# Performance work log

Hardware: AMD Instinct MI355X
Metric: run time of the kernel (lower is better)

Reference implementation:

```python
import jax, jax.numpy as jnp
import numpy as np
from jax import lax

B, S, I, H = 64, 512, 1024, 1024


def _lstm_dir(x, W_ih, W_hh, b_ih, b_hh):
    # x: [B, S, I] -> hidden states [B, S, H]
    # Precompute input projections for all timesteps in one GEMM.
    xg = jnp.einsum('bsi,gi->bsg', x, W_ih) + b_ih + b_hh  # [B, S, 4H]
    Whh_T = W_hh.T  # [H, 4H]
    h0 = jnp.zeros((x.shape[0], W_hh.shape[1]), dtype=x.dtype)
    c0 = jnp.zeros_like(h0)

    def step(carry, xg_t):
        h, c = carry
        g = xg_t + h @ Whh_T  # [B, 4H]
        i_g, f_g, g_g, o_g = jnp.split(g, 4, axis=-1)  # PyTorch gate order i,f,g,o
        i_g = jax.nn.sigmoid(i_g)
        f_g = jax.nn.sigmoid(f_g)
        g_g = jnp.tanh(g_g)
        o_g = jax.nn.sigmoid(o_g)
        c = f_g * c + i_g * g_g
        h = o_g * jnp.tanh(c)
        return (h, c), h

    _, hs = lax.scan(step, (h0, c0), jnp.swapaxes(xg, 0, 1))  # hs: [S, B, H]
    return jnp.swapaxes(hs, 0, 1)


def setup_inputs() -> dict:
    key = jax.random.key(0)
    ks = jax.random.split(key, 10)
    s = 1.0 / np.sqrt(H)  # PyTorch LSTMCell init scale
    return {
        'forward_x': jax.random.normal(ks[0], (B, S, I), jnp.float32),
        'backward_x': jax.random.normal(ks[1], (B, S, I), jnp.float32),
        'W_ih_f': jax.random.uniform(ks[2], (4 * H, I), jnp.float32, -s, s),
        'W_hh_f': jax.random.uniform(ks[3], (4 * H, H), jnp.float32, -s, s),
        'b_ih_f': jax.random.uniform(ks[4], (4 * H,), jnp.float32, -s, s),
        'b_hh_f': jax.random.uniform(ks[5], (4 * H,), jnp.float32, -s, s),
        'W_ih_b': jax.random.uniform(ks[6], (4 * H, I), jnp.float32, -s, s),
        'W_hh_b': jax.random.uniform(ks[7], (4 * H, H), jnp.float32, -s, s),
        'b_ih_b': jax.random.uniform(ks[8], (4 * H,), jnp.float32, -s, s),
        'b_hh_b': jax.random.uniform(ks[9], (4 * H,), jnp.float32, -s, s),
    }


def reference(forward_x, backward_x, W_ih_f, W_hh_f, b_ih_f, b_hh_f,
              W_ih_b, W_hh_b, b_ih_b, b_hh_b):
    fwd = _lstm_dir(forward_x, W_ih_f, W_hh_f, b_ih_f, b_hh_f)
    # Backward direction consumes backward_x from the last timestep to the
    # first and writes hidden states back at their original positions,
    # i.e. run on the time-reversed sequence and reverse the outputs.
    bwd = _lstm_dir(backward_x[:, ::-1, :], W_ih_b, W_hh_b, b_ih_b, b_hh_b)[:, ::-1, :]
    return fwd, bwd
```

## Files before the change

kernel.cpp:

```cpp
#include <hip/hip_runtime.h>
#include <hip/hip_bf16.h>
#include <cstdint>


typedef __bf16 bf16_t;
typedef bf16_t bf16x8 __attribute__((ext_vector_type(8)));
typedef float  f32x4  __attribute__((ext_vector_type(4)));
typedef int    i32x2  __attribute__((ext_vector_type(2)));

#define DEVI __device__ __forceinline__

constexpr int Bb = 64, Ss = 512, Ii = 1024, Hh = 1024;
constexpr size_t WS_FLAGS  = 0;
constexpr size_t WS_HRING  = 4096;
constexpr size_t WS_XBF    = 1ull << 20;
constexpr size_t XBF_BYTES = 2ull * Ss * Bb * Ii * 2;
constexpr size_t WS_NEED_XBF = WS_XBF + XBF_BYTES;
constexpr int LDS_TOTAL = 163840;

DEVI float fast_sig(float x) {
  float z = __expf(-fabsf(x));
  float r = __builtin_amdgcn_rcpf(1.f + z);
  return x >= 0.f ? r : z * r;
}
DEVI float fast_tanh(float x) {
  float z = __expf(-2.f * fabsf(x));
  float r = (1.f - z) * __builtin_amdgcn_rcpf(1.f + z);
  return x >= 0.f ? r : -r;
}
DEVI bf16x8 cvt8(f32x4 a, f32x4 b) {
  bf16x8 r;
  r[0] = (bf16_t)a[0]; r[1] = (bf16_t)a[1]; r[2] = (bf16_t)a[2]; r[3] = (bf16_t)a[3];
  r[4] = (bf16_t)b[0]; r[5] = (bf16_t)b[1]; r[6] = (bf16_t)b[2]; r[7] = (bf16_t)b[3];
  return r;
}
DEVI uint32_t pk_bf16(float lo, float hi) {
  union { bf16_t b[2]; uint32_t u; } x;
  x.b[0] = (bf16_t)lo; x.b[1] = (bf16_t)hi;
  return x.u;
}
DEVI f32x4 mfma16(bf16x8 a, bf16x8 b, f32x4 c) {
  return __builtin_amdgcn_mfma_f32_16x16x32_bf16(a, b, c, 0, 0, 0);
}

#define GLDS16(g, s)                                                           \
  __builtin_amdgcn_global_load_lds(                                            \
      (const __attribute__((address_space(1))) void*)(const void*)(g),         \
      (__attribute__((address_space(3))) void*)(void*)(s), 16, 0, 0)
#define GLDS16_COH(g, s)                                                       \
  __builtin_amdgcn_global_load_lds(                                            \
      (const __attribute__((address_space(1))) void*)(const void*)(g),         \
      (__attribute__((address_space(3))) void*)(void*)(s), 16, 0, 17)
#define WAIT_LGKM0 asm volatile("s_waitcnt lgkmcnt(0)" ::: "memory")
#define WAIT_VM0   asm volatile("s_waitcnt vmcnt(0)" ::: "memory")
#define BARRIER_RAW                                                            \
  do { __builtin_amdgcn_s_barrier(); __builtin_amdgcn_sched_barrier(0); } while (0)

__global__ void k_init(int* flags) {
  int i = threadIdx.x;
  if (i < 256) flags[i] = 0;
}

__global__ void k_convx(const float* __restrict__ xf, const float* __restrict__ xb,
                        bf16_t* __restrict__ dst) {
  size_t og = (size_t)blockIdx.x * blockDim.x + threadIdx.x;
  int i8  = (int)(og & 127);
  int b   = (int)((og >> 7) & 63);
  int t   = (int)((og >> 13) & 511);
  int dir = (int)(og >> 22);
  const float* src = (dir ? xb : xf) + (((size_t)b * Ss + t) * Ii + (size_t)i8 * 8);
  f32x4 a = *(const f32x4*)src;
  f32x4 c = *(const f32x4*)(src + 4);
  *(bf16x8*)(dst + og * 8) = cvt8(a, c);
}

template <bool XBF>
__global__ void __launch_bounds__(512, 2)
k_lstm(const float* __restrict__ xf, const float* __restrict__ xb,
       const float* __restrict__ Wih_f, const float* __restrict__ Whh_f,
       const float* __restrict__ bih_f, const float* __restrict__ bhh_f,
       const float* __restrict__ Wih_b, const float* __restrict__ Whh_b,
       const float* __restrict__ bih_b, const float* __restrict__ bhh_b,
       float* __restrict__ out,
       const bf16_t* __restrict__ xbfin, bf16_t* __restrict__ hring,
       int* __restrict__ flags) {
  extern __shared__ char lds[];
  char* PA = lds;
  char* PB = lds + 65536;
  float* part = (float*)(lds + 131072);

  const int tid = threadIdx.x;
  const int bid = blockIdx.x;
  const int dir = bid & 1;
  const int db  = bid >> 1;
  const int n0  = db * 8;
  const int w   = tid >> 6, l = tid & 63;
  const int u   = l >> 4, l15 = l & 15;
  const int m   = w & 1;
  const int kq  = w >> 1;

  const float* Wih = dir ? Wih_b : Wih_f;
  const float* Whh = dir ? Whh_b : Whh_f;
  const float* bih = dir ? bih_b : bih_f;
  const float* bhh = dir ? bhh_b : bhh_f;
  const float* x32 = dir ? xb : xf;
  const bf16_t* xbase = xbfin + (size_t)dir * Ss * Bb * Ii;
  bf16_t* hr = hring + (size_t)dir * 2 * Bb * Hh;
  float* outD = out + (size_t)dir * Bb * Ss * Hh;
  int* myflags = flags + dir * 128;

  bf16x8 wr[2][2][4][2];
#pragma unroll
  for (int mat = 0; mat < 2; ++mat)
#pragma unroll
    for (int p = 0; p < 2; ++p)
#pragma unroll
      for (int ks = 0; ks < 4; ++ks)
#pragma unroll
        for (int nt = 0; nt < 2; ++nt) {
          int c = nt * 16 + l15;
          int j = (c >> 3) * 1024 + n0 + (c & 7);
          int k = p * 512 + kq * 128 + ks * 32 + u * 8;
          const float* sp = (mat ? Whh : Wih) + (size_t)j * 1024 + k;
          wr[mat][p][ks][nt] = cvt8(*(const f32x4*)sp, *(const f32x4*)(sp + 4));
        }

  const int eb = tid >> 3, en = tid & 7;
  const int nj = n0 + en;
  float bi0 = bih[nj] + bhh[nj];
  float bi1 = bih[1024 + nj] + bhh[1024 + nj];
  float bi2 = bih[2048 + nj] + bhh[2048 + nj];
  float bi3 = bih[3072 + nj] + bhh[3072 + nj];

  int aoff0[4], aoff1[4];
#pragma unroll
  for (int ks = 0; ks < 4; ++ks) {
    int r0 = m * 32 + l15;
    int r1 = r0 + 16;
    int sl = kq * 16 + ks * 4 + u;
    aoff0[ks] = r0 * 1024 + ((sl ^ (r0 & 7)) << 4);
    aoff1[ks] = r1 * 1024 + ((sl ^ (r1 & 7)) << 4);
  }

  auto STAGE_DMA = [&](char* panel, const bf16_t* srcb) {
#pragma unroll
    for (int i = 0; i < 8; ++i) {
      const bf16_t* gp = srcb + (size_t)(w * 8 + i) * 1024 + ((l ^ i) << 3);
      GLDS16(gp, panel + (w * 8 + i) * 1024);
    }
  };
  auto STAGE_H = [&](char* panel, const bf16_t* srcb) {
#pragma unroll
    for (int i = 0; i < 8; ++i) {
      const bf16_t* gp = srcb + (size_t)(w * 8 + i) * 1024 + ((l ^ i) << 3);
      GLDS16_COH(gp, panel + (w * 8 + i) * 1024);
    }
  };
  auto STAGE_XF = [&](char* panel, const float* srcb) {
#pragma unroll
    for (int i = 0; i < 8; ++i) {
      int r = w * 8 + i;
      const float* sp = srcb + (size_t)r * (Ss * Ii) + ((l ^ i) << 3);
      f32x4 a = *(const f32x4*)sp;
      f32x4 b = *(const f32x4*)(sp + 4);
      *(bf16x8*)(panel + r * 1024 + l * 16) = cvt8(a, b);
    }
  };

  f32x4 acc00, acc01, acc10, acc11;
#define COMPUTE(panel, matC, pC)                                               \
  do {                                                                         \
    _Pragma("unroll") for (int ks = 0; ks < 4; ++ks) {                         \
      bf16x8 a0_ = *(const bf16x8*)((panel) + aoff0[ks]);                      \
      bf16x8 a1_ = *(const bf16x8*)((panel) + aoff1[ks]);                      \
      acc00 = mfma16(a0_, wr[matC][pC][ks][0], acc00);                         \
      acc01 = mfma16(a0_, wr[matC][pC][ks][1], acc01);                         \
      acc10 = mfma16(a1_, wr[matC][pC][ks][0], acc10);                         \
      acc11 = mfma16(a1_, wr[matC][pC][ks][1], acc11);                         \
    }                                                                          \
  } while (0)

  float c_reg = 0.f;

  {
    int t0 = dir ? (Ss - 1) : 0;
    if constexpr (XBF) {
      STAGE_DMA(PA, xbase + (size_t)t0 * (Bb * Ii));
      STAGE_DMA(PB, xbase + (size_t)t0 * (Bb * Ii) + 512);
    } else {
      STAGE_XF(PA, x32 + (size_t)t0 * Ii);
      STAGE_XF(PB, x32 + (size_t)t0 * Ii + 512);
    }
  }

  for (int step = 0; step < Ss; ++step) {
    const int t  = dir ? (Ss - 1 - step) : step;
    const int tn = dir ? (Ss - 2 - step) : (step + 1);
    const bf16_t* hbase = hr + (size_t)((step - 1) & 1) * (Bb * Hh);

    WAIT_VM0; WAIT_LGKM0; BARRIER_RAW;

    acc00 = f32x4{0.f, 0.f, 0.f, 0.f}; acc01 = acc00; acc10 = acc00; acc11 = acc00;

    COMPUTE(PA, 0, 0);
    COMPUTE(PB, 0, 1);
    WAIT_LGKM0;

    if (step > 0 && w == 0) {
      const int* fp = &myflags[l * 2];
      for (;;) {
        i32x2 f;
        asm volatile("global_load_dwordx2 %0, %1, off sc0 sc1\n\t"
                     "s_waitcnt vmcnt(0)"
                     : "=v"(f) : "v"((uint64_t)fp) : "memory");
        if (__ballot((f[0] < step) || (f[1] < step)) == 0ull) break;
        __builtin_amdgcn_s_sleep(1);
      }
    }
    BARRIER_RAW;

    if (step > 0) {
      STAGE_H(PA, hbase);
      STAGE_H(PB, hbase + 512);
      WAIT_VM0; BARRIER_RAW;
      COMPUTE(PA, 1, 0);
      COMPUTE(PB, 1, 1);
      WAIT_LGKM0;
    }

#pragma unroll
    for (int rr = 0; rr < 2; ++rr)
#pragma unroll
      for (int nt = 0; nt < 2; ++nt) {
        f32x4 a = (rr == 0) ? (nt == 0 ? acc00 : acc01) : (nt == 0 ? acc10 : acc11);
#pragma unroll
        for (int q = 0; q < 4; ++q) {
          int R = m * 32 + rr * 16 + u * 4 + q;
          int C = nt * 16 + l15;
          part[(kq * 64 + R) * 32 + (C ^ ((R & 7) << 2))] = a[q];
        }
      }
    WAIT_LGKM0; BARRIER_RAW;

    float hval;
    {
      const int sk = (eb & 7) << 2;
      float g0 = bi0, g1 = bi1, g2 = bi2, g3 = bi3;
#pragma unroll
      for (int q = 0; q < 4; ++q) {
        const float* pp = &part[(q * 64 + eb) * 32];
        g0 += pp[en ^ sk]; g1 += pp[(8 + en) ^ sk];
        g2 += pp[(16 + en) ^ sk]; g3 += pp[(24 + en) ^ sk];
      }
      float ig = fast_sig(g0), fg = fast_sig(g1);
      float gg = fast_tanh(g2), og = fast_sig(g3);
      c_reg = fg * c_reg + ig * gg;
      hval = og * fast_tanh(c_reg);
      uint32_t p01 = pk_bf16(hval, __shfl_xor(hval, 1));
      uint32_t p23 = __shfl_xor(p01, 2);
      if ((en & 3) == 0) {
        uint64_t q8 = (uint64_t)p01 | ((uint64_t)p23 << 32);
        uint64_t* dst = (uint64_t*)&hr[(size_t)(step & 1) * (Bb * Hh) +
                                       (size_t)eb * Hh + n0 + (en & 4)];
        __hip_atomic_store(dst, q8, __ATOMIC_RELAXED, __HIP_MEMORY_SCOPE_AGENT);
      }
    }

    WAIT_VM0; BARRIER_RAW;
    if (tid == 0) {
      __hip_atomic_store(&myflags[db], step + 1, __ATOMIC_RELAXED,
                         __HIP_MEMORY_SCOPE_AGENT);
    }

    outD[(size_t)eb * (Ss * Hh) + (size_t)t * Hh + n0 + en] = hval;
    if (step < Ss - 1) {
      if constexpr (XBF) {
        STAGE_DMA(PA, xbase + (size_t)tn * (Bb * Ii));
        STAGE_DMA(PB, xbase + (size_t)tn * (Bb * Ii) + 512);
      } else {
        STAGE_XF(PA, x32 + (size_t)tn * Ii);
        STAGE_XF(PB, x32 + (size_t)tn * Ii + 512);
      }
    }
  }
#undef COMPUTE
}

extern "C" void kernel_launch(void* const* d_in, const int* in_sizes, int n_in,
                              void* d_out, int out_size, void* d_ws, size_t ws_size,
                              hipStream_t stream) {
  (void)in_sizes; (void)n_in; (void)out_size;
  const float* xf    = (const float*)d_in[0];
  const float* xb    = (const float*)d_in[1];
  const float* Wih_f = (const float*)d_in[2];
  const float* Whh_f = (const float*)d_in[3];
  const float* bih_f = (const float*)d_in[4];
  const float* bhh_f = (const float*)d_in[5];
  const float* Wih_b = (const float*)d_in[6];
  const float* Whh_b = (const float*)d_in[7];
  const float* bih_b = (const float*)d_in[8];
  const float* bhh_b = (const float*)d_in[9];
  float* outp = (float*)d_out;
  char* ws = (char*)d_ws;
  int* flagsp = (int*)(ws + WS_FLAGS);
  bf16_t* hringp = (bf16_t*)(ws + WS_HRING);
  const bf16_t* xbfp = (const bf16_t*)(ws + WS_XBF);
  const bool use_xbf = ws_size >= WS_NEED_XBF;

  hipLaunchKernelGGL(k_init, dim3(1), dim3(256), 0, stream, flagsp);
  if (use_xbf) {
    hipLaunchKernelGGL(k_convx, dim3(32768), dim3(256), 0, stream,
                       xf, xb, (bf16_t*)(ws + WS_XBF));
  }

  void* args[] = {&xf, &xb, &Wih_f, &Whh_f, &bih_f, &bhh_f,
                  &Wih_b, &Whh_b, &bih_b, &bhh_b,
                  &outp, &xbfp, &hringp, &flagsp};
  using KFn = void (*)(const float*, const float*, const float*, const float*,
                       const float*, const float*, const float*, const float*,
                       const float*, const float*, float*, const bf16_t*,
                       bf16_t*, int*);
  KFn kp = use_xbf ? (KFn)k_lstm<true> : (KFn)k_lstm<false>;
  hipFuncSetAttribute((const void*)kp, hipFuncAttributeMaxDynamicSharedMemorySize,
                      LDS_TOTAL);
  hipLaunchCooperativeKernel((const void*)kp, dim3(256), dim3(512), args,
                             LDS_TOTAL, stream);
}
```

Before: 3.712 ms.

## Load x operands directly into registers and simplify flag polling

Replaces LDS staging of the per-step x tile (DMA or fp32 convert into LDS panels) with direct global loads into a 16-entry bf16x8 register array that feeds the MFMA input projection, so the x path no longer needs LDS traffic or the barrier at the top of each step. The next step's x is prefetched into registers at the end of the current step. Flag polling changes from one wavefront doing dwordx2 loads with ballot and sleep to 128 threads each spinning on a single flag with relaxed atomic loads. The workspace offset for the bf16 x copy is also moved. The cost is much higher register pressure, and the busy-spin without sleep adds memory polling traffic.

Result: slower. 5.872 ms (+58.2%).

```diff
diff --git a/kernel.cpp b/kernel.cpp
--- a/kernel.cpp
+++ b/kernel.cpp
@@ -6,14 +6,13 @@
 typedef __bf16 bf16_t;
 typedef bf16_t bf16x8 __attribute__((ext_vector_type(8)));
 typedef float  f32x4  __attribute__((ext_vector_type(4)));
-typedef int    i32x2  __attribute__((ext_vector_type(2)));
 
 #define DEVI __device__ __forceinline__
 
 constexpr int Bb = 64, Ss = 512, Ii = 1024, Hh = 1024;
 constexpr size_t WS_FLAGS  = 0;
 constexpr size_t WS_HRING  = 4096;
-constexpr size_t WS_XBF    = 1ull << 20;
+constexpr size_t WS_XBF    = 528384;
 constexpr size_t XBF_BYTES = 2ull * Ss * Bb * Ii * 2;
 constexpr size_t WS_NEED_XBF = WS_XBF + XBF_BYTES;
 constexpr int LDS_TOTAL = 163840;
@@ -43,10 +42,6 @@
   return __builtin_amdgcn_mfma_f32_16x16x32_bf16(a, b, c, 0, 0, 0);
 }
 
-#define GLDS16(g, s)                                                           \
-  __builtin_amdgcn_global_load_lds(                                            \
-      (const __attribute__((address_space(1))) void*)(const void*)(g),         \
-      (__attribute__((address_space(3))) void*)(void*)(s), 16, 0, 0)
 #define GLDS16_COH(g, s)                                                       \
   __builtin_amdgcn_global_load_lds(                                            \
       (const __attribute__((address_space(1))) void*)(const void*)(g),         \
@@ -142,13 +137,6 @@
     aoff1[ks] = r1 * 1024 + ((sl ^ (r1 & 7)) << 4);
   }
 
-  auto STAGE_DMA = [&](char* panel, const bf16_t* srcb) {
-#pragma unroll
-    for (int i = 0; i < 8; ++i) {
-      const bf16_t* gp = srcb + (size_t)(w * 8 + i) * 1024 + ((l ^ i) << 3);
-      GLDS16(gp, panel + (w * 8 + i) * 1024);
-    }
-  };
   auto STAGE_H = [&](char* panel, const bf16_t* srcb) {
 #pragma unroll
     for (int i = 0; i < 8; ++i) {
@@ -156,65 +144,71 @@
       GLDS16_COH(gp, panel + (w * 8 + i) * 1024);
     }
   };
-  auto STAGE_XF = [&](char* panel, const float* srcb) {
-#pragma unroll
-    for (int i = 0; i < 8; ++i) {
-      int r = w * 8 + i;
-      const float* sp = srcb + (size_t)r * (Ss * Ii) + ((l ^ i) << 3);
-      f32x4 a = *(const f32x4*)sp;
-      f32x4 b = *(const f32x4*)(sp + 4);
-      *(bf16x8*)(panel + r * 1024 + l * 16) = cvt8(a, b);
-    }
+
+  bf16x8 xa[16];
+  const int xr0 = m * 32 + l15;
+  auto LOADX = [&](int tt) {
+#pragma unroll
+    for (int p = 0; p < 2; ++p)
+#pragma unroll
+      for (int ks = 0; ks < 4; ++ks)
+#pragma unroll
+        for (int r01 = 0; r01 < 2; ++r01) {
+          int row = xr0 + r01 * 16;
+          int k = p * 512 + kq * 128 + ks * 32 + u * 8;
+          if constexpr (XBF) {
+            xa[p * 8 + ks * 2 + r01] =
+                *(const bf16x8*)(xbase + (size_t)tt * (Bb * Ii) +
+                                 (size_t)row * 1024 + k);
+          } else {
+            const float* sp = x32 + ((size_t)row * Ss + tt) * Ii + k;
+            xa[p * 8 + ks * 2 + r01] =
+                cvt8(*(const f32x4*)sp, *(const f32x4*)(sp + 4));
+          }
+        }
   };
 
   f32x4 acc00, acc01, acc10, acc11;
-#define COMPUTE(panel, matC, pC)                                               \
+#define COMPX                                                                  \
+  do {                                                                         \
+    _Pragma("unroll") for (int p = 0; p < 2; ++p)                              \
+    _Pragma("unroll") for (int ks = 0; ks < 4; ++ks) {                         \
+      bf16x8 a0_ = xa[p * 8 + ks * 2 + 0];                                     \
+      bf16x8 a1_ = xa[p * 8 + ks * 2 + 1];                                     \
+      acc00 = mfma16(a0_, wr[0][p][ks][0], acc00);                             \
+      acc01 = mfma16(a0_, wr[0][p][ks][1], acc01);                             \
+      acc10 = mfma16(a1_, wr[0][p][ks][0], acc10);                             \
+      acc11 = mfma16(a1_, wr[0][p][ks][1], acc11);                             \
+    }                                                                          \
+  } while (0)
+#define COMPH(panel, pC)                                                       \
   do {                                                                         \
     _Pragma("unroll") for (int ks = 0; ks < 4; ++ks) {                         \
       bf16x8 a0_ = *(const bf16x8*)((panel) + aoff0[ks]);                      \
       bf16x8 a1_ = *(const bf16x8*)((panel) + aoff1[ks]);                      \
-      acc00 = mfma16(a0_, wr[matC][pC][ks][0], acc00);                         \
-      acc01 = mfma16(a0_, wr[matC][pC][ks][1], acc01);                         \
-      acc10 = mfma16(a1_, wr[matC][pC][ks][0], acc10);                         \
-      acc11 = mfma16(a1_, wr[matC][pC][ks][1], acc11);                         \
+      acc00 = mfma16(a0_, wr[1][pC][ks][0], acc00);                            \
+      acc01 = mfma16(a0_, wr[1][pC][ks][1], acc01);                            \
+      acc10 = mfma16(a1_, wr[1][pC][ks][0], acc10);                            \
+      acc11 = mfma16(a1_, wr[1][pC][ks][1], acc11);                            \
     }                                                                          \
   } while (0)
 
   float c_reg = 0.f;
 
-  {
-    int t0 = dir ? (Ss - 1) : 0;
-    if constexpr (XBF) {
-      STAGE_DMA(PA, xbase + (size_t)t0 * (Bb * Ii));
-      STAGE_DMA(PB, xbase + (size_t)t0 * (Bb * Ii) + 512);
-    } else {
-      STAGE_XF(PA, x32 + (size_t)t0 * Ii);
-      STAGE_XF(PB, x32 + (size_t)t0 * Ii + 512);
-    }
-  }
+  LOADX(dir ? (Ss - 1) : 0);
 
   for (int step = 0; step < Ss; ++step) {
     const int t  = dir ? (Ss - 1 - step) : step;
     const int tn = dir ? (Ss - 2 - step) : (step + 1);
     const bf16_t* hbase = hr + (size_t)((step - 1) & 1) * (Bb * Hh);
 
-    WAIT_VM0; WAIT_LGKM0; BARRIER_RAW;
-
     acc00 = f32x4{0.f, 0.f, 0.f, 0.f}; acc01 = acc00; acc10 = acc00; acc11 = acc00;
 
-    COMPUTE(PA, 0, 0);
-    COMPUTE(PB, 0, 1);
-    WAIT_LGKM0;
-
-    if (step > 0 && w == 0) {
-      const int* fp = &myflags[l * 2];
-      for (;;) {
-        i32x2 f;
-        asm volatile("global_load_dwordx2 %0, %1, off sc0 sc1\n\t"
-                     "s_waitcnt vmcnt(0)"
-                     : "=v"(f) : "v"((uint64_t)fp) : "memory");
-        if (__ballot((f[0] < step) || (f[1] < step)) == 0ull) break;
-        __builtin_amdgcn_s_sleep(1);
+    COMPX;
+
+    if (step > 0 && tid < 128) {
+      const int* fp = &myflags[tid];
+      while (__hip_atomic_load(fp, __ATOMIC_RELAXED, __HIP_MEMORY_SCOPE_AGENT) < step) {
       }
     }
     BARRIER_RAW;
@@ -223,8 +217,8 @@
       STAGE_H(PA, hbase);
       STAGE_H(PB, hbase + 512);
       WAIT_VM0; BARRIER_RAW;
-      COMPUTE(PA, 1, 0);
-      COMPUTE(PB, 1, 1);
+      COMPH(PA, 0);
+      COMPH(PB, 1);
       WAIT_LGKM0;
     }
 
@@ -273,17 +267,10 @@
     }
 
     outD[(size_t)eb * (Ss * Hh) + (size_t)t * Hh + n0 + en] = hval;
-    if (step < Ss - 1) {
-      if constexpr (XBF) {
-        STAGE_DMA(PA, xbase + (size_t)tn * (Bb * Ii));
-        STAGE_DMA(PB, xbase + (size_t)tn * (Bb * Ii) + 512);
-      } else {
-        STAGE_XF(PA, x32 + (size_t)tn * Ii);
-        STAGE_XF(PB, x32 + (size_t)tn * Ii + 512);
-      }
-    }
+    if (step < Ss - 1) LOADX(tn);
   }
-#undef COMPUTE
+#undef COMPX
+#undef COMPH
 }
 
 extern "C" void kernel_launch(void* const* d_in, const int* in_sizes, int n_in,
```

## Fuse x bf16 conversion into recurrent kernel via rolling lookahead window

Applied to the files above, without the earlier changes.

Removes the separate k_convx pre-pass that converted the full fp32 input to bf16 for all timesteps. Blocks with db<64 each convert one batch row of x a few steps ahead (LA=4) into an 8-slot ring buffer, overlapping that work with the recurrence. An initial flag barrier is added and all blocks stage x panels from the ring. The flag polling also changes from a single wave with a ballot and s_sleep to 128 threads spinning on relaxed atomic loads. This risks extra load traffic in the critical step loop and depends on the per-step flag barrier to order ring reuse.

Measured after the change: 3.266 ms. 1.14x faster.

```diff
diff --git a/kernel.cpp b/kernel.cpp
--- a/kernel.cpp
+++ b/kernel.cpp
@@ -6,16 +6,16 @@
 typedef __bf16 bf16_t;
 typedef bf16_t bf16x8 __attribute__((ext_vector_type(8)));
 typedef float  f32x4  __attribute__((ext_vector_type(4)));
-typedef int    i32x2  __attribute__((ext_vector_type(2)));
 
 #define DEVI __device__ __forceinline__
 
 constexpr int Bb = 64, Ss = 512, Ii = 1024, Hh = 1024;
-constexpr size_t WS_FLAGS  = 0;
-constexpr size_t WS_HRING  = 4096;
-constexpr size_t WS_XBF    = 1ull << 20;
-constexpr size_t XBF_BYTES = 2ull * Ss * Bb * Ii * 2;
-constexpr size_t WS_NEED_XBF = WS_XBF + XBF_BYTES;
+constexpr int W = 8, LA = 4;
+constexpr size_t WS_FLAGS = 0;
+constexpr size_t WS_HRING = 4096;
+constexpr size_t WS_XWIN  = 528384;
+constexpr size_t XWIN_BYTES = 2ull * W * Bb * Ii * 2;
+constexpr size_t WS_NEED_XW = WS_XWIN + XWIN_BYTES;
 constexpr int LDS_TOTAL = 163840;
 
 DEVI float fast_sig(float x) {
@@ -43,10 +43,6 @@
   return __builtin_amdgcn_mfma_f32_16x16x32_bf16(a, b, c, 0, 0, 0);
 }
 
-#define GLDS16(g, s)                                                           \
-  __builtin_amdgcn_global_load_lds(                                            \
-      (const __attribute__((address_space(1))) void*)(const void*)(g),         \
-      (__attribute__((address_space(3))) void*)(void*)(s), 16, 0, 0)
 #define GLDS16_COH(g, s)                                                       \
   __builtin_amdgcn_global_load_lds(                                            \
       (const __attribute__((address_space(1))) void*)(const void*)(g),         \
@@ -58,23 +54,10 @@
 
 __global__ void k_init(int* flags) {
   int i = threadIdx.x;
-  if (i < 256) flags[i] = 0;
-}
-
-__global__ void k_convx(const float* __restrict__ xf, const float* __restrict__ xb,
-                        bf16_t* __restrict__ dst) {
-  size_t og = (size_t)blockIdx.x * blockDim.x + threadIdx.x;
-  int i8  = (int)(og & 127);
-  int b   = (int)((og >> 7) & 63);
-  int t   = (int)((og >> 13) & 511);
-  int dir = (int)(og >> 22);
-  const float* src = (dir ? xb : xf) + (((size_t)b * Ss + t) * Ii + (size_t)i8 * 8);
-  f32x4 a = *(const f32x4*)src;
-  f32x4 c = *(const f32x4*)(src + 4);
-  *(bf16x8*)(dst + og * 8) = cvt8(a, c);
-}
-
-template <bool XBF>
+  if (i < 256) flags[i] = -1;
+}
+
+template <bool XW>
 __global__ void __launch_bounds__(512, 2)
 k_lstm(const float* __restrict__ xf, const float* __restrict__ xb,
        const float* __restrict__ Wih_f, const float* __restrict__ Whh_f,
@@ -82,7 +65,7 @@
        const float* __restrict__ Wih_b, const float* __restrict__ Whh_b,
        const float* __restrict__ bih_b, const float* __restrict__ bhh_b,
        float* __restrict__ out,
-       const bf16_t* __restrict__ xbfin, bf16_t* __restrict__ hring,
+       bf16_t* __restrict__ xw, bf16_t* __restrict__ hring,
        int* __restrict__ flags) {
   extern __shared__ char lds[];
   char* PA = lds;
@@ -104,8 +87,8 @@
   const float* bih = dir ? bih_b : bih_f;
   const float* bhh = dir ? bhh_b : bhh_f;
   const float* x32 = dir ? xb : xf;
-  const bf16_t* xbase = xbfin + (size_t)dir * Ss * Bb * Ii;
   bf16_t* hr = hring + (size_t)dir * 2 * Bb * Hh;
+  bf16_t* xwd = xw + (size_t)dir * W * Bb * Ii;
   float* outD = out + (size_t)dir * Bb * Ss * Hh;
   int* myflags = flags + dir * 128;
 
@@ -142,14 +125,7 @@
     aoff1[ks] = r1 * 1024 + ((sl ^ (r1 & 7)) << 4);
   }
 
-  auto STAGE_DMA = [&](char* panel, const bf16_t* srcb) {
-#pragma unroll
-    for (int i = 0; i < 8; ++i) {
-      const bf16_t* gp = srcb + (size_t)(w * 8 + i) * 1024 + ((l ^ i) << 3);
-      GLDS16(gp, panel + (w * 8 + i) * 1024);
-    }
-  };
-  auto STAGE_H = [&](char* panel, const bf16_t* srcb) {
+  auto STAGE_P = [&](char* panel, const bf16_t* srcb) {
 #pragma unroll
     for (int i = 0; i < 8; ++i) {
       const bf16_t* gp = srcb + (size_t)(w * 8 + i) * 1024 + ((l ^ i) << 3);
@@ -181,16 +157,38 @@
   } while (0)
 
   float c_reg = 0.f;
-
-  {
+  const bool conv = XW && (db < 64);
+
+  if constexpr (XW) {
+    if (conv) {
+#pragma unroll
+      for (int s0 = 0; s0 < LA; ++s0) {
+        int tc = dir ? (Ss - 1 - s0) : s0;
+        float2 cv = *(const float2*)(x32 + ((size_t)db * Ss + tc) * Ii + tid * 2);
+        uint32_t* dst = (uint32_t*)(xwd + (size_t)s0 * (Bb * Ii) + db * 1024 + tid * 2);
+        __hip_atomic_store(dst, pk_bf16(cv.x, cv.y), __ATOMIC_RELAXED,
+                           __HIP_MEMORY_SCOPE_AGENT);
+      }
+    }
+    WAIT_VM0;
+  }
+  BARRIER_RAW;
+  if (tid == 0) {
+    __hip_atomic_store(&myflags[db], 0, __ATOMIC_RELAXED, __HIP_MEMORY_SCOPE_AGENT);
+  }
+  if (tid < 128) {
+    const int* fp = &myflags[tid];
+    while (__hip_atomic_load(fp, __ATOMIC_RELAXED, __HIP_MEMORY_SCOPE_AGENT) < 0) {
+    }
+  }
+  BARRIER_RAW;
+  if constexpr (XW) {
+    STAGE_P(PA, xwd);
+    STAGE_P(PB, xwd + 512);
+  } else {
     int t0 = dir ? (Ss - 1) : 0;
-    if constexpr (XBF) {
-      STAGE_DMA(PA, xbase + (size_t)t0 * (Bb * Ii));
-      STAGE_DMA(PB, xbase + (size_t)t0 * (Bb * Ii) + 512);
-    } else {
-      STAGE_XF(PA, x32 + (size_t)t0 * Ii);
-      STAGE_XF(PB, x32 + (size_t)t0 * Ii + 512);
-    }
+    STAGE_XF(PA, x32 + (size_t)t0 * Ii);
+    STAGE_XF(PB, x32 + (size_t)t0 * Ii + 512);
   }
 
   for (int step = 0; step < Ss; ++step) {
@@ -200,28 +198,29 @@
 
     WAIT_VM0; WAIT_LGKM0; BARRIER_RAW;
 
+    float2 cx;
+    const bool cnow = conv && (step + LA) < Ss;
+    if (cnow) {
+      int tc = dir ? (Ss - 1 - (step + LA)) : (step + LA);
+      cx = *(const float2*)(x32 + ((size_t)db * Ss + tc) * Ii + tid * 2);
+    }
+
     acc00 = f32x4{0.f, 0.f, 0.f, 0.f}; acc01 = acc00; acc10 = acc00; acc11 = acc00;
 
     COMPUTE(PA, 0, 0);
     COMPUTE(PB, 0, 1);
     WAIT_LGKM0;
 
-    if (step > 0 && w == 0) {
-      const int* fp = &myflags[l * 2];
-      for (;;) {
-        i32x2 f;
-        asm volatile("global_load_dwordx2 %0, %1, off sc0 sc1\n\t"
-                     "s_waitcnt vmcnt(0)"
-                     : "=v"(f) : "v"((uint64_t)fp) : "memory");
-        if (__ballot((f[0] < step) || (f[1] < step)) == 0ull) break;
-        __builtin_amdgcn_s_sleep(1);
+    if (step > 0 && tid < 128) {
+      const int* fp = &myflags[tid];
+      while (__hip_atomic_load(fp, __ATOMIC_RELAXED, __HIP_MEMORY_SCOPE_AGENT) < step) {
       }
     }
     BARRIER_RAW;
 
     if (step > 0) {
-      STAGE_H(PA, hbase);
-      STAGE_H(PB, hbase + 512);
+      STAGE_P(PA, hbase);
+      STAGE_P(PB, hbase + 512);
       WAIT_VM0; BARRIER_RAW;
       COMPUTE(PA, 1, 0);
       COMPUTE(PB, 1, 1);
@@ -265,6 +264,12 @@
         __hip_atomic_store(dst, q8, __ATOMIC_RELAXED, __HIP_MEMORY_SCOPE_AGENT);
       }
     }
+    if (cnow) {
+      uint32_t* dst = (uint32_t*)(xwd + (size_t)((step + LA) & (W - 1)) * (Bb * Ii) +
+                                  db * 1024 + tid * 2);
+      __hip_atomic_store(dst, pk_bf16(cx.x, cx.y), __ATOMIC_RELAXED,
+                         __HIP_MEMORY_SCOPE_AGENT);
+    }
 
     WAIT_VM0; BARRIER_RAW;
     if (tid == 0) {
@@ -274,9 +279,10 @@
 
     outD[(size_t)eb * (Ss * Hh) + (size_t)t * Hh + n0 + en] = hval;
     if (step < Ss - 1) {
-      if constexpr (XBF) {
-        STAGE_DMA(PA, xbase + (size_t)tn * (Bb * Ii));
-        STAGE_DMA(PB, xbase + (size_t)tn * (Bb * Ii) + 512);
+      if constexpr (XW) {
+        const bf16_t* wsl = xwd + (size_t)((step + 1) & (W - 1)) * (Bb * Ii);
+        STAGE_P(PA, wsl);
+        STAGE_P(PB, wsl + 512);
       } else {
         STAGE_XF(PA, x32 + (size_t)tn * Ii);
         STAGE_XF(PB, x32 + (size_t)tn * Ii + 512);
@@ -304,23 +310,19 @@
   char* ws = (char*)d_ws;
   int* flagsp = (int*)(ws + WS_FLAGS);
   bf16_t* hringp = (bf16_t*)(ws + WS_HRING);
-  const bf16_t* xbfp = (const bf16_t*)(ws + WS_XBF);
-  const bool use_xbf = ws_size >= WS_NEED_XBF;
+  bf16_t* xwp = (bf16_t*)(ws + WS_XWIN);
+  const bool use_xw = ws_size >= WS_NEED_XW;
 
   hipLaunchKernelGGL(k_init, dim3(1), dim3(256), 0, stream, flagsp);
-  if (use_xbf) {
-    hipLaunchKernelGGL(k_convx, dim3(32768), dim3(256), 0, stream,
-                       xf, xb, (bf16_t*)(ws + WS_XBF));
-  }
 
   void* args[] = {&xf, &xb, &Wih_f, &Whh_f, &bih_f, &bhh_f,
                   &Wih_b, &Whh_b, &bih_b, &bhh_b,
-                  &outp, &xbfp, &hringp, &flagsp};
+                  &outp, &xwp, &hringp, &flagsp};
   using KFn = void (*)(const float*, const float*, const float*, const float*,
                        const float*, const float*, const float*, const float*,
-                       const float*, const float*, float*, const bf16_t*,
+                       const float*, const float*, float*, bf16_t*,
                        bf16_t*, int*);
-  KFn kp = use_xbf ? (KFn)k_lstm<true> : (KFn)k_lstm<false>;
+  KFn kp = use_xw ? (KFn)k_lstm<true> : (KFn)k_lstm<false>;
   hipFuncSetAttribute((const void*)kp, hipFuncAttributeMaxDynamicSharedMemorySize,
                       LDS_TOTAL);
   hipLaunchCooperativeKernel((const void*)kp, dim3(256), dim3(512), args,
```
